# Kernel optimization log

Measured on AMD Instinct MI355X. Metric: run time of the kernel, lower is better.

## Reference

```python
import jax, jax.numpy as jnp
import numpy as np

N_SENT = 2048      # total sentences
SEQ_L = 128        # words per sentence
D = 256            # encoder_output_dim
C = 64             # num_classes
NUM_BAGS = 128     # number of ragged scopes (here 16 sentences each)


def setup_inputs() -> dict:
    key = jax.random.key(0)
    k1, k2, k3, k4, k5, k6 = jax.random.split(key, 6)
    x = jax.random.normal(k1, (N_SENT, SEQ_L, D), dtype=jnp.float32)
    attention_query = jax.random.randint(k2, (N_SENT,), 0, C, dtype=jnp.int64)
    # scope offsets [0,16,32,...] expressed as per-sentence segment ids
    seg_ids = jnp.repeat(jnp.arange(NUM_BAGS, dtype=jnp.int64), N_SENT // NUM_BAGS)
    relation_W = jax.random.normal(k3, (C, D), dtype=jnp.float32) * 0.05
    attention_W = jax.random.normal(k4, (C, D), dtype=jnp.float32) * 0.05
    assemble_W = jax.random.normal(k5, (C, D * D), dtype=jnp.float32) * 0.02
    bias = jax.random.normal(k6, (C,), dtype=jnp.float32)
    return {"x": x, "attention_query": attention_query, "seg_ids": seg_ids,
            "relation_W": relation_W, "attention_W": attention_W,
            "assemble_W": assemble_W, "bias": bias}


def reference(x, attention_query, seg_ids, relation_W, attention_W, assemble_W, bias):
    n = x.shape[0]
    rq = relation_W[attention_query]                       # [n, d]
    A = assemble_W[attention_query].reshape(n, D, D)       # [n, d, d]
    # word-relation alignment attention: bmm(bmm(x, A), rq)
    xa = jnp.einsum('nld,nde->nle', x, A)                  # [n, L, d]
    att_logits = jnp.einsum('nle,ne->nl', xa, rq)          # [n, L]
    att_w = jax.nn.softmax(att_logits, axis=1)             # softmax over words
    x_pool = jnp.einsum('nl,nld->nd', att_w, x)            # [n, d]

    # sentence-level bag attention logit
    att_b = attention_W[attention_query]                   # [n, d]
    logit = jnp.sum(x_pool * att_b * rq, axis=1)           # [n]

    # ragged per-bag softmax over sentences (replaces Python loop over scope)
    m = jax.ops.segment_max(logit, seg_ids, num_segments=NUM_BAGS)
    e = jnp.exp(logit - m[seg_ids])
    den = jax.ops.segment_sum(e, seg_ids, num_segments=NUM_BAGS)
    w = e / den[seg_ids]                                   # [n]
    repre = jax.ops.segment_sum(w[:, None] * x_pool, seg_ids, num_segments=NUM_BAGS)  # [B, d]

    # dropout with p=0 is identity
    logits = repre @ relation_W.T + bias                   # [B, C]
    return logits
```

## Files before the change

kernel.cpp:

```cpp
#include <hip/hip_runtime.h>
#include <hip/hip_bf16.h>

#define N_SENT   2048
#define SEQ_L    128
#define DIM      256
#define NCLS     64
#define NUM_BAGS 128
#define SENT_PER_BAG 16

__global__ __launch_bounds__(1024) void fix_query(
    const int* __restrict__ qraw, int* __restrict__ qfix)
{
    __shared__ int s_flag;
    int t = threadIdx.x;
    if (t == 0) s_flag = 0;
    __syncthreads();
    if (qraw[2 * t + 1] != 0) atomicOr(&s_flag, 1);
    __syncthreads();
    int is_int32 = s_flag;
    for (int n = t; n < N_SENT; n += 1024)
        qfix[n] = (is_int32 ? qraw[n] : qraw[2 * n]) & 63;
}

__global__ __launch_bounds__(256) void precompute_vb(
    const float* __restrict__ relW, const float* __restrict__ attW,
    const float* __restrict__ asmW, float* __restrict__ v, float* __restrict__ b)
{
    int c = blockIdx.x >> 2;
    int quarter = blockIdx.x & 3;
    int t = threadIdx.x;
    int wid = t >> 6, lane = t & 63;

    __shared__ float s_rq[DIM];
    s_rq[t] = relW[c * DIM + t];
    if (quarter == 0) b[c * DIM + t] = relW[c * DIM + t] * attW[c * DIM + t];
    __syncthreads();

    float4 rq4 = ((const float4*)s_rq)[lane];
    const float* base = asmW + (size_t)c * DIM * DIM;
    for (int i = 0; i < 16; ++i) {
        int d = quarter * 64 + wid * 16 + i;
        float4 a4 = *(const float4*)(base + (size_t)d * DIM + lane * 4);
        float s = a4.x * rq4.x + a4.y * rq4.y + a4.z * rq4.z + a4.w * rq4.w;
        #pragma unroll
        for (int o = 32; o > 0; o >>= 1) s += __shfl_xor(s, o);
        if (lane == 0) v[c * DIM + d] = s;
    }
}

__global__ __launch_bounds__(256) void sentence_kernel(
    const float* __restrict__ x, const int* __restrict__ qidx,
    const float* __restrict__ v, const float* __restrict__ b,
    float* __restrict__ x_pool, float* __restrict__ sent_logit)
{
    int n = blockIdx.x;
    int t = threadIdx.x;
    int wid = t >> 6, lane = t & 63;
    int q = qidx[n];

    __shared__ float s_log[SEQ_L];
    __shared__ float s_m, s_inv;
    __shared__ float s_pool[4 * DIM];
    __shared__ float s_red[4];

    const float* xs = x + (size_t)n * SEQ_L * DIM;
    float4 vr = ((const float4*)(v + q * DIM))[lane];

    for (int j = 0; j < 32; ++j) {
        int l = wid * 32 + j;
        float4 xv = *(const float4*)(xs + (size_t)l * DIM + lane * 4);
        float s = xv.x * vr.x + xv.y * vr.y + xv.z * vr.z + xv.w * vr.w;
        #pragma unroll
        for (int o = 32; o > 0; o >>= 1) s += __shfl_xor(s, o);
        if (lane == 0) s_log[l] = s;
    }
    __syncthreads();

    if (wid == 0) {
        float a0 = s_log[lane], a1 = s_log[lane + 64];
        float m = fmaxf(a0, a1);
        #pragma unroll
        for (int o = 32; o > 0; o >>= 1) m = fmaxf(m, __shfl_xor(m, o));
        float e = expf(a0 - m) + expf(a1 - m);
        #pragma unroll
        for (int o = 32; o > 0; o >>= 1) e += __shfl_xor(e, o);
        if (lane == 0) { s_m = m; s_inv = 1.f / e; }
    }
    __syncthreads();
    float m = s_m, inv = s_inv;

    float4 acc = make_float4(0.f, 0.f, 0.f, 0.f);
    for (int j = 0; j < 32; ++j) {
        int l = wid * 32 + j;
        float wl = expf(s_log[l] - m) * inv;
        float4 xv = *(const float4*)(xs + (size_t)l * DIM + lane * 4);
        acc.x += wl * xv.x; acc.y += wl * xv.y;
        acc.z += wl * xv.z; acc.w += wl * xv.w;
    }
    ((float4*)(s_pool + wid * DIM))[lane] = acc;
    __syncthreads();

    float xp = s_pool[t] + s_pool[DIM + t] + s_pool[2 * DIM + t] + s_pool[3 * DIM + t];
    x_pool[(size_t)n * DIM + t] = xp;
    float p = xp * b[q * DIM + t];
    #pragma unroll
    for (int o = 32; o > 0; o >>= 1) p += __shfl_xor(p, o);
    if (lane == 0) s_red[wid] = p;
    __syncthreads();
    if (t == 0) sent_logit[n] = s_red[0] + s_red[1] + s_red[2] + s_red[3];
}

__global__ __launch_bounds__(64) void bag_kernel(
    const float* __restrict__ sent_logit, const float* __restrict__ x_pool,
    const float* __restrict__ relW, const float* __restrict__ bias,
    float* __restrict__ out)
{
    int bg = blockIdx.x;
    int lane = threadIdx.x;
    __shared__ float s_rep[DIM];
    int n0 = bg * SENT_PER_BAG;

    float lg[SENT_PER_BAG];
    float m = -1e30f;
    #pragma unroll
    for (int i = 0; i < SENT_PER_BAG; ++i) {
        lg[i] = sent_logit[n0 + i];
        m = fmaxf(m, lg[i]);
    }
    float den = 0.f;
    #pragma unroll
    for (int i = 0; i < SENT_PER_BAG; ++i) { lg[i] = expf(lg[i] - m); den += lg[i]; }
    float inv = 1.f / den;

    float4 rep = make_float4(0.f, 0.f, 0.f, 0.f);
    #pragma unroll
    for (int i = 0; i < SENT_PER_BAG; ++i) {
        float w = lg[i] * inv;
        float4 xp = *(const float4*)(x_pool + (size_t)(n0 + i) * DIM + lane * 4);
        rep.x += w * xp.x; rep.y += w * xp.y; rep.z += w * xp.z; rep.w += w * xp.w;
    }
    ((float4*)s_rep)[lane] = rep;
    __syncthreads();

    const float4* row = (const float4*)(relW + lane * DIM);
    const float4* rp  = (const float4*)s_rep;
    float acc = bias[lane];
    #pragma unroll 8
    for (int j = 0; j < DIM / 4; ++j) {
        float4 w4 = row[j];
        float4 r4 = rp[j];
        acc += w4.x * r4.x + w4.y * r4.y + w4.z * r4.z + w4.w * r4.w;
    }
    out[bg * NCLS + lane] = acc;
}

extern "C" void kernel_launch(void* const* d_in, const int* in_sizes, int n_in,
                              void* d_out, int out_size, void* d_ws, size_t ws_size,
                              hipStream_t stream) {
    const float* x    = (const float*)d_in[0];
    const int*   qraw = (const int*)d_in[1];
    const float* relW = (const float*)d_in[3];
    const float* attW = (const float*)d_in[4];
    const float* asmW = (const float*)d_in[5];
    const float* bias = (const float*)d_in[6];
    float* out = (float*)d_out;

    char* ws = (char*)d_ws;
    float* v  = (float*)ws;
    float* b  = (float*)(ws + (64 * 256 * 4));
    float* sl = (float*)(ws + (2 * 64 * 256 * 4));
    float* xp = (float*)(ws + (2 * 64 * 256 * 4) + 2048 * 4);
    int*   qf = (int*)(ws + (2 * 64 * 256 * 4) + 2048 * 4 + (size_t)N_SENT * DIM * 4);

    fix_query<<<1, 1024, 0, stream>>>(qraw, qf);
    precompute_vb<<<NCLS * 4, 256, 0, stream>>>(relW, attW, asmW, v, b);
    sentence_kernel<<<N_SENT, 256, 0, stream>>>(x, qf, v, b, xp, sl);
    bag_kernel<<<NUM_BAGS, 64, 0, stream>>>(sl, xp, relW, bias, out);
}
```

Baseline: 421.5 us.

## Hold sentence x tile in registers, precompute softmax weights, fold query fix into precompute

```diff
diff --git a/kernel.cpp b/kernel.cpp
--- a/kernel.cpp
+++ b/kernel.cpp
@@ -8,23 +8,10 @@
 #define NUM_BAGS 128
 #define SENT_PER_BAG 16
 
-__global__ __launch_bounds__(1024) void fix_query(
-    const int* __restrict__ qraw, int* __restrict__ qfix)
-{
-    __shared__ int s_flag;
-    int t = threadIdx.x;
-    if (t == 0) s_flag = 0;
-    __syncthreads();
-    if (qraw[2 * t + 1] != 0) atomicOr(&s_flag, 1);
-    __syncthreads();
-    int is_int32 = s_flag;
-    for (int n = t; n < N_SENT; n += 1024)
-        qfix[n] = (is_int32 ? qraw[n] : qraw[2 * n]) & 63;
-}
-
 __global__ __launch_bounds__(256) void precompute_vb(
     const float* __restrict__ relW, const float* __restrict__ attW,
-    const float* __restrict__ asmW, float* __restrict__ v, float* __restrict__ b)
+    const float* __restrict__ asmW, const int* __restrict__ qraw,
+    float* __restrict__ v, float* __restrict__ b, int* __restrict__ qfix)
 {
     int c = blockIdx.x >> 2;
     int quarter = blockIdx.x & 3;
@@ -32,9 +19,13 @@
     int wid = t >> 6, lane = t & 63;
 
     __shared__ float s_rq[DIM];
+    __shared__ int s_flag;
+    if (t == 0) s_flag = 0;
     s_rq[t] = relW[c * DIM + t];
     if (quarter == 0) b[c * DIM + t] = relW[c * DIM + t] * attW[c * DIM + t];
     __syncthreads();
+
+    if (t < 8 && qraw[2 * t + 1] != 0) atomicOr(&s_flag, 1);
 
     float4 rq4 = ((const float4*)s_rq)[lane];
     const float* base = asmW + (size_t)c * DIM * DIM;
@@ -45,6 +36,12 @@
         #pragma unroll
         for (int o = 32; o > 0; o >>= 1) s += __shfl_xor(s, o);
         if (lane == 0) v[c * DIM + d] = s;
+    }
+
+    __syncthreads();
+    if (t < 8) {
+        int i = blockIdx.x * 8 + t;
+        qfix[i] = (s_flag ? qraw[i] : qraw[2 * i]) & 63;
     }
 }
 
@@ -59,20 +56,25 @@
     int q = qidx[n];
 
     __shared__ float s_log[SEQ_L];
-    __shared__ float s_m, s_inv;
+    __shared__ float s_w[SEQ_L];
     __shared__ float s_pool[4 * DIM];
     __shared__ float s_red[4];
 
-    const float* xs = x + (size_t)n * SEQ_L * DIM;
+    const float* xs = x + (size_t)n * SEQ_L * DIM
+                        + (size_t)wid * 32 * DIM + lane * 4;
     float4 vr = ((const float4*)(v + q * DIM))[lane];
 
+    float4 xv[32];
+    #pragma unroll
+    for (int j = 0; j < 32; ++j)
+        xv[j] = *(const float4*)(xs + (size_t)j * DIM);
+
+    #pragma unroll
     for (int j = 0; j < 32; ++j) {
-        int l = wid * 32 + j;
-        float4 xv = *(const float4*)(xs + (size_t)l * DIM + lane * 4);
-        float s = xv.x * vr.x + xv.y * vr.y + xv.z * vr.z + xv.w * vr.w;
+        float s = xv[j].x * vr.x + xv[j].y * vr.y + xv[j].z * vr.z + xv[j].w * vr.w;
         #pragma unroll
         for (int o = 32; o > 0; o >>= 1) s += __shfl_xor(s, o);
-        if (lane == 0) s_log[l] = s;
+        if (lane == 0) s_log[wid * 32 + j] = s;
     }
     __syncthreads();
 
@@ -81,21 +83,22 @@
         float m = fmaxf(a0, a1);
         #pragma unroll
         for (int o = 32; o > 0; o >>= 1) m = fmaxf(m, __shfl_xor(m, o));
-        float e = expf(a0 - m) + expf(a1 - m);
+        float e0 = expf(a0 - m), e1 = expf(a1 - m);
+        float e = e0 + e1;
         #pragma unroll
         for (int o = 32; o > 0; o >>= 1) e += __shfl_xor(e, o);
-        if (lane == 0) { s_m = m; s_inv = 1.f / e; }
+        float inv = 1.f / e;
+        s_w[lane] = e0 * inv;
+        s_w[lane + 64] = e1 * inv;
     }
     __syncthreads();
-    float m = s_m, inv = s_inv;
 
     float4 acc = make_float4(0.f, 0.f, 0.f, 0.f);
+    #pragma unroll
     for (int j = 0; j < 32; ++j) {
-        int l = wid * 32 + j;
-        float wl = expf(s_log[l] - m) * inv;
-        float4 xv = *(const float4*)(xs + (size_t)l * DIM + lane * 4);
-        acc.x += wl * xv.x; acc.y += wl * xv.y;
-        acc.z += wl * xv.z; acc.w += wl * xv.w;
+        float wl = s_w[wid * 32 + j];
+        acc.x += wl * xv[j].x; acc.y += wl * xv[j].y;
+        acc.z += wl * xv[j].z; acc.w += wl * xv[j].w;
     }
     ((float4*)(s_pool + wid * DIM))[lane] = acc;
     __syncthreads();
@@ -172,8 +175,7 @@
     float* xp = (float*)(ws + (2 * 64 * 256 * 4) + 2048 * 4);
     int*   qf = (int*)(ws + (2 * 64 * 256 * 4) + 2048 * 4 + (size_t)N_SENT * DIM * 4);
 
-    fix_query<<<1, 1024, 0, stream>>>(qraw, qf);
-    precompute_vb<<<NCLS * 4, 256, 0, stream>>>(relW, attW, asmW, v, b);
+    precompute_vb<<<NCLS * 4, 256, 0, stream>>>(relW, attW, asmW, qraw, v, b, qf);
     sentence_kernel<<<N_SENT, 256, 0, stream>>>(x, qf, v, b, xp, sl);
     bag_kernel<<<NUM_BAGS, 64, 0, stream>>>(sl, xp, relW, bias, out);
 }
```

After: 394.6 us. -6.4%, faster.
